# Optimization experiments

Hardware: AMD Instinct MI355X
Metric: run time of the kernel (lower is better)

Reference implementation:

```python
import jax, jax.numpy as jnp
import numpy as np

N = 50000  # nodes
E = 800000  # edges (avg degree 16)


def gcn_agg(x, senders, receivers, n, add_self_edges):
    """jraph.GraphConvolution aggregation with symmetric normalization.
    x: [n, d] node feats already passed through update_node_fn."""
    if add_self_edges:
        idx = jnp.arange(n, dtype=senders.dtype)
        s = jnp.concatenate([senders, idx])
        r = jnp.concatenate([receivers, idx])
    else:
        s, r = senders, receivers
    ones = jnp.ones(s.shape, x.dtype)
    sdeg = jax.ops.segment_sum(ones, s, num_segments=n)
    rdeg = jax.ops.segment_sum(ones, r, num_segments=n)
    x = x * jax.lax.rsqrt(jnp.maximum(sdeg, 1.0))[:, None]
    x = jax.ops.segment_sum(x[s], r, num_segments=n)  # [E+,d] gather -> scatter-sum
    return x * jax.lax.rsqrt(jnp.maximum(rdeg, 1.0))[:, None]


def setup_inputs() -> dict:
    key = jax.random.key(0)
    ks = jax.random.split(key, 9)
    d_in, d_h, d_z, d_out = 128, 128, 64, 128

    def w(k, i, o):
        return jax.random.normal(k, (i, o), jnp.float32) / np.float32(np.sqrt(i))

    return {
        "nodes": jax.random.normal(ks[0], (N, d_in), jnp.float32),
        "senders": jax.random.randint(ks[1], (E,), 0, N, jnp.int32),
        "receivers": jax.random.randint(ks[2], (E,), 0, N, jnp.int32),
        "eps": jax.random.normal(ks[3], (N, d_z), jnp.float32),
        "W_h": w(ks[4], d_in, d_h), "b_h": jnp.zeros((d_h,), jnp.float32),
        "W_mu": w(ks[5], d_h, d_z), "b_mu": jnp.zeros((d_z,), jnp.float32),
        "W_ls": w(ks[6], d_h, d_z), "b_ls": jnp.zeros((d_z,), jnp.float32),
        "W_dh": w(ks[7], d_z, d_h), "b_dh": jnp.zeros((d_h,), jnp.float32),
        "W_do": w(ks[8], d_h, d_out), "b_do": jnp.zeros((d_out,), jnp.float32),
    }


def reference(nodes, senders, receivers, eps, W_h, b_h, W_mu, b_mu,
              W_ls, b_ls, W_dh, b_dh, W_do, b_do):
    n = nodes.shape[0]
    # encoder hidden GCN (add_self_edges=True): Linear+elu update, then agg.
    # (the first of the two identical encoder GCN calls in the source is dead
    #  code -- both read the original graph, only the 2nd result is used)
    h = jax.nn.elu(nodes @ W_h + b_h)
    h = gcn_agg(h, senders, receivers, n, True)
    # mean / log_std GCNs (add_self_edges=False)
    mean = gcn_agg(h @ W_mu + b_mu, senders, receivers, n, False)
    log_std = gcn_agg(h @ W_ls + b_ls, senders, receivers, n, False)
    # reparameterization
    z = mean + jnp.exp(log_std) * eps
    # decoder: GCN(self edges, Linear+elu) -> GCN(no self edges, Linear)
    d = jax.nn.elu(z @ W_dh + b_dh)
    d = gcn_agg(d, senders, receivers, n, True)
    out = gcn_agg(d @ W_do + b_do, senders, receivers, n, False)
    return mean, log_std, out
```

## Files before the change

### kernel.cpp

```cpp
#include <hip/hip_runtime.h>
#include <hip/hip_bf16.h>
#include <hip/hip_fp16.h>
#include <math.h>


typedef _Float16 f16x8 __attribute__((ext_vector_type(8)));
typedef float    f32x4 __attribute__((ext_vector_type(4)));

#define HSL 128
#define HIST_LDS_W 12544

__global__ __launch_bounds__(256)
void hist8_k(const int* __restrict__ snd, const int* __restrict__ rcv,
             unsigned int* __restrict__ partial, int nE, int nW)
{
    __shared__ unsigned int sh[HIST_LDS_W];
    const int slice = blockIdx.x, arr = blockIdx.y;
    const int* __restrict__ idx = arr ? rcv : snd;
    for (int w = threadIdx.x; w < nW; w += 256) sh[w] = 0u;
    __syncthreads();
    const int per = (nE + HSL - 1) / HSL;
    const int e1 = min(nE, slice * per + per);
    for (int e = slice * per + threadIdx.x; e < e1; e += 256) {
        int v = idx[e];
        atomicAdd(&sh[v >> 2], 1u << ((v & 3) * 8));
    }
    __syncthreads();
    unsigned int* dst = partial + ((size_t)arr * HSL + slice) * nW;
    for (int w = threadIdx.x; w < nW; w += 256) dst[w] = sh[w];
}

__global__ __launch_bounds__(256)
void hist8_reduce_k(const unsigned int* __restrict__ partial, int* __restrict__ rdeg,
                    float* __restrict__ dsi, float* __restrict__ dri,
                    float* __restrict__ dsn, float* __restrict__ drn,
                    int n, int nW)
{
    int gid = blockIdx.x * 256 + threadIdx.x;
    if (gid >= 2 * nW) return;
    const int arr = gid / nW, w = gid % nW;
    const unsigned int* src = partial + (size_t)arr * HSL * nW + w;
    int c0 = 0, c1 = 0, c2 = 0, c3 = 0;
    for (int s = 0; s < HSL; ++s) {
        unsigned int v = src[(size_t)s * nW];
        c0 += v & 255u; c1 += (v >> 8) & 255u; c2 += (v >> 16) & 255u; c3 += v >> 24;
    }
    const int cc[4] = {c0, c1, c2, c3};
    const int node0 = w * 4;
#pragma unroll
    for (int u = 0; u < 4; ++u) {
        int node = node0 + u;
        if (node >= n) break;
        float fd = (float)cc[u];
        if (arr == 0) {
            dsi[node] = rsqrtf(fd + 1.0f);
            dsn[node] = rsqrtf(fmaxf(fd, 1.0f));
        } else {
            rdeg[node] = cc[u];
            dri[node] = rsqrtf(fd + 1.0f);
            drn[node] = rsqrtf(fmaxf(fd, 1.0f));
        }
    }
}

__global__ __launch_bounds__(256)
void scan_part_k(const int* __restrict__ deg, int* __restrict__ partial, int n)
{
    __shared__ int sh[256];
    const int t = threadIdx.x;
    const int i = blockIdx.x * 1024 + t * 4;
    int s = 0;
    if (i + 3 < n) { int4 v = *(const int4*)&deg[i]; s = v.x + v.y + v.z + v.w; }
    else { for (int u = 0; u < 4; u++) if (i + u < n) s += deg[i + u]; }
    sh[t] = s; __syncthreads();
    for (int off = 128; off > 0; off >>= 1) {
        if (t < off) sh[t] += sh[t + off];
        __syncthreads();
    }
    if (t == 0) partial[blockIdx.x] = sh[0];
}

__global__ __launch_bounds__(256)
void scan_mid_k(int* __restrict__ partial, int nb, int* __restrict__ row_start, int n)
{
    __shared__ int sh[256];
    const int t = threadIdx.x;
    int v = (t < nb) ? partial[t] : 0;
    sh[t] = v; __syncthreads();
#pragma unroll
    for (int off = 1; off < 256; off <<= 1) {
        int u = (t >= off) ? sh[t - off] : 0;
        __syncthreads();
        sh[t] += u;
        __syncthreads();
    }
    if (t < nb) partial[t] = sh[t];
    if (t == 255) row_start[n] = sh[255];
}

__global__ __launch_bounds__(256)
void scan_apply_k(const int* __restrict__ deg, const int* __restrict__ partial,
                  int* __restrict__ row_start, int* __restrict__ cursor, int n)
{
    __shared__ int sh[256];
    const int t = threadIdx.x;
    const int b = blockIdx.x;
    const int i = b * 1024 + t * 4;
    const int boff = (b == 0) ? 0 : partial[b - 1];
    int v0 = 0, v1 = 0, v2 = 0, v3 = 0;
    if (i + 3 < n) { int4 v = *(const int4*)&deg[i]; v0 = v.x; v1 = v.y; v2 = v.z; v3 = v.w; }
    else {
        if (i     < n) v0 = deg[i];
        if (i + 1 < n) v1 = deg[i + 1];
        if (i + 2 < n) v2 = deg[i + 2];
        if (i + 3 < n) v3 = deg[i + 3];
    }
    const int ts = v0 + v1 + v2 + v3;
    sh[t] = ts; __syncthreads();
#pragma unroll
    for (int off = 1; off < 256; off <<= 1) {
        int u = (t >= off) ? sh[t - off] : 0;
        __syncthreads();
        sh[t] += u;
        __syncthreads();
    }
    const int excl = boff + sh[t] - ts;
    const int p0 = excl, p1 = p0 + v0, p2 = p1 + v1, p3 = p2 + v2;
    if (i + 3 < n) {
        *(int4*)&row_start[i] = make_int4(p0, p1, p2, p3);
        *(int4*)&cursor[i]    = make_int4(p0, p1, p2, p3);
    } else {
        if (i     < n) { row_start[i]     = p0; cursor[i]     = p0; }
        if (i + 1 < n) { row_start[i + 1] = p1; cursor[i + 1] = p1; }
        if (i + 2 < n) { row_start[i + 2] = p2; cursor[i + 2] = p2; }
        if (i + 3 < n) { row_start[i + 3] = p3; cursor[i + 3] = p3; }
    }
}

__global__ __launch_bounds__(256)
void fill_csr_k(const int* __restrict__ s, const int* __restrict__ r,
                int* __restrict__ cursor, int* __restrict__ csr, int nE)
{
    int e = blockIdx.x * 256 + threadIdx.x;
    if (e < nE) {
        int pos = atomicAdd(&cursor[r[e]], 1);
        csr[pos] = s[e];
    }
}

__global__ __launch_bounds__(256)
void wprep_k(const float* __restrict__ W_h, const float* __restrict__ W_mu,
             const float* __restrict__ W_ls, const float* __restrict__ W_dh,
             const float* __restrict__ W_do,
             const float* __restrict__ b_mu, const float* __restrict__ b_ls,
             __half* __restrict__ WT_h, __half* __restrict__ WT2,
             __half* __restrict__ WT_dh, __half* __restrict__ WT_do,
             float* __restrict__ bias2)
{
    int gid = blockIdx.x * 256 + threadIdx.x;
    if (gid < 16384) {
        int m = gid >> 7, k = gid & 127;
        WT_h[gid] = __float2half(W_h[k * 128 + m]);
    } else if (gid < 32768) {
        int t = gid - 16384; int m = t >> 7, k = t & 127;
        float v = (m < 64) ? W_mu[k * 64 + m] : W_ls[k * 64 + (m - 64)];
        WT2[t] = __float2half(v);
    } else if (gid < 40960) {
        int t = gid - 32768; int m = t >> 6, k = t & 63;
        WT_dh[t] = __float2half(W_dh[k * 128 + m]);
    } else if (gid < 57344) {
        int t = gid - 40960; int m = t >> 7, k = t & 127;
        WT_do[t] = __float2half(W_do[k * 128 + m]);
    } else if (gid < 57472) {
        int c = gid - 57344;
        bias2[c] = (c < 64) ? b_mu[c] : b_ls[c - 64];
    }
}

template<int K, int ELU, typename XT>
__global__ __launch_bounds__(256)
void mgemm_k(const XT* __restrict__ X, const __half* __restrict__ WT,
             const float* __restrict__ Bias, const float* __restrict__ rowscale,
             __half* __restrict__ Y, int nrows)
{
    const int lane = threadIdx.x & 63;
    const int w    = threadIdx.x >> 6;
    const int l15  = lane & 15, l4 = lane >> 4;
    const int rowbase = blockIdx.x * 128 + w * 32;
    if (rowbase >= nrows) return;

    f32x4 acc[2][8];
#pragma unroll
    for (int mt = 0; mt < 2; ++mt)
#pragma unroll
        for (int nt = 0; nt < 8; ++nt)
#pragma unroll
            for (int q = 0; q < 4; ++q) acc[mt][nt][q] = 0.f;

    const int r0 = min(rowbase + l15,      nrows - 1);
    const int r1 = min(rowbase + 16 + l15, nrows - 1);

#pragma unroll
    for (int ks = 0; ks < K / 32; ++ks) {
        const int ko = ks * 32 + l4 * 8;
        f16x8 a0, a1;
        if constexpr (sizeof(XT) == 4) {
            const float4 p0 = *(const float4*)&X[(size_t)r0 * K + ko];
            const float4 p1 = *(const float4*)&X[(size_t)r0 * K + ko + 4];
            const float4 q0 = *(const float4*)&X[(size_t)r1 * K + ko];
            const float4 q1 = *(const float4*)&X[(size_t)r1 * K + ko + 4];
            a0[0] = (_Float16)p0.x; a0[1] = (_Float16)p0.y;
            a0[2] = (_Float16)p0.z; a0[3] = (_Float16)p0.w;
            a0[4] = (_Float16)p1.x; a0[5] = (_Float16)p1.y;
            a0[6] = (_Float16)p1.z; a0[7] = (_Float16)p1.w;
            a1[0] = (_Float16)q0.x; a1[1] = (_Float16)q0.y;
            a1[2] = (_Float16)q0.z; a1[3] = (_Float16)q0.w;
            a1[4] = (_Float16)q1.x; a1[5] = (_Float16)q1.y;
            a1[6] = (_Float16)q1.z; a1[7] = (_Float16)q1.w;
        } else {
            a0 = *(const f16x8*)&X[(size_t)r0 * K + ko];
            a1 = *(const f16x8*)&X[(size_t)r1 * K + ko];
        }
#pragma unroll
        for (int nt = 0; nt < 8; ++nt) {
            const f16x8 b = *(const f16x8*)&WT[(size_t)(nt * 16 + l15) * K + ko];
            acc[0][nt] = __builtin_amdgcn_mfma_f32_16x16x32_f16(a0, b, acc[0][nt], 0, 0, 0);
            acc[1][nt] = __builtin_amdgcn_mfma_f32_16x16x32_f16(a1, b, acc[1][nt], 0, 0, 0);
        }
    }

    float rs[2][4]; int gr[2][4];
#pragma unroll
    for (int mt = 0; mt < 2; ++mt)
#pragma unroll
        for (int i = 0; i < 4; ++i) {
            int g = rowbase + mt * 16 + l4 * 4 + i;
            gr[mt][i] = g;
            rs[mt][i] = (g < nrows) ? rowscale[g] : 0.f;
        }
#pragma unroll
    for (int nt = 0; nt < 8; ++nt) {
        const float bias = Bias[nt * 16 + l15];
#pragma unroll
        for (int mt = 0; mt < 2; ++mt)
#pragma unroll
            for (int i = 0; i < 4; ++i) {
                if (gr[mt][i] < nrows) {
                    float v = acc[mt][nt][i] + bias;
                    if (ELU) v = (v > 0.f) ? v : expm1f(v);
                    Y[(size_t)gr[mt][i] * 128 + nt * 16 + l15] = __float2half(v * rs[mt][i]);
                }
            }
    }
}

__device__ inline void agg_core(const __half* __restrict__ y, const int* __restrict__ csr,
                                int beg, int end, int g, int c16, float (&acc)[8])
{
    int j = beg;
    for (; j + 8 <= end; j += 8) {
        const int s0 = csr[j + g], s1 = csr[j + 4 + g];
        const f16x8 r0 = *(const f16x8*)&y[(size_t)s0 * 128 + c16 * 8];
        const f16x8 r1 = *(const f16x8*)&y[(size_t)s1 * 128 + c16 * 8];
#pragma unroll
        for (int k = 0; k < 8; ++k) acc[k] += (float)r0[k] + (float)r1[k];
    }
    for (; j < end; j += 4) {
        const int e = j + g;
        const bool ok = e < end;
        const int s = csr[ok ? e : end - 1];
        const f16x8 r = *(const f16x8*)&y[(size_t)s * 128 + c16 * 8];
        if (ok) {
#pragma unroll
            for (int k = 0; k < 8; ++k) acc[k] += (float)r[k];
        }
    }
#pragma unroll
    for (int k = 0; k < 8; ++k) {
        acc[k] += __shfl_xor(acc[k], 16);
        acc[k] += __shfl_xor(acc[k], 32);
    }
}

__global__ __launch_bounds__(256)
void aggw_self_k(const __half* __restrict__ y, const int* __restrict__ row_start,
                 const int* __restrict__ csr, const float* __restrict__ rsc,
                 __half* __restrict__ out, int n)
{
    const int v    = (blockIdx.x * 256 + threadIdx.x) >> 6;
    const int lane = threadIdx.x & 63;
    if (v >= n) return;
    const int g = lane >> 4, c16 = lane & 15;
    const int beg = row_start[v], end = row_start[v + 1];

    float acc[8] = {0.f, 0.f, 0.f, 0.f, 0.f, 0.f, 0.f, 0.f};
    if (g == 0) {
        const f16x8 r = *(const f16x8*)&y[(size_t)v * 128 + c16 * 8];
#pragma unroll
        for (int k = 0; k < 8; ++k) acc[k] += (float)r[k];
    }
    agg_core(y, csr, beg, end, g, c16, acc);
    if (g == 0) {
        const float sc = rsc[v];
        f16x8 o;
#pragma unroll
        for (int k = 0; k < 8; ++k) o[k] = (_Float16)(acc[k] * sc);
        *(f16x8*)&out[(size_t)v * 128 + c16 * 8] = o;
    }
}

__global__ __launch_bounds__(256)
void aggw_f32_k(const __half* __restrict__ y, const int* __restrict__ row_start,
                const int* __restrict__ csr, const float* __restrict__ rsc,
                float* __restrict__ out, int n)
{
    const int v    = (blockIdx.x * 256 + threadIdx.x) >> 6;
    const int lane = threadIdx.x & 63;
    if (v >= n) return;
    const int g = lane >> 4, c16 = lane & 15;
    const int beg = row_start[v], end = row_start[v + 1];

    float acc[8] = {0.f, 0.f, 0.f, 0.f, 0.f, 0.f, 0.f, 0.f};
    agg_core(y, csr, beg, end, g, c16, acc);
    const float sc = rsc[v];
    if (g == 0)
        *(float4*)&out[(size_t)v * 128 + c16 * 8] =
            make_float4(acc[0] * sc, acc[1] * sc, acc[2] * sc, acc[3] * sc);
    if (g == 1)
        *(float4*)&out[(size_t)v * 128 + c16 * 8 + 4] =
            make_float4(acc[4] * sc, acc[5] * sc, acc[6] * sc, acc[7] * sc);
}

__global__ __launch_bounds__(256)
void aggw_2z_k(const __half* __restrict__ y, const int* __restrict__ row_start,
               const int* __restrict__ csr, const float* __restrict__ rsc,
               const float* __restrict__ eps,
               float* __restrict__ mean, float* __restrict__ lstd,
               __half* __restrict__ z16, int n)
{
    const int v    = (blockIdx.x * 256 + threadIdx.x) >> 6;
    const int lane = threadIdx.x & 63;
    if (v >= n) return;
    const int g = lane >> 4, c16 = lane & 15;
    const int beg = row_start[v], end = row_start[v + 1];

    float acc[8] = {0.f, 0.f, 0.f, 0.f, 0.f, 0.f, 0.f, 0.f};
    agg_core(y, csr, beg, end, g, c16, acc);
    const float sc = rsc[v];
#pragma unroll
    for (int k = 0; k < 8; ++k) acc[k] *= sc;

    if (c16 < 8) {
        if (g == 0) *(float4*)&mean[(size_t)v * 64 + c16 * 8]     = make_float4(acc[0], acc[1], acc[2], acc[3]);
        if (g == 1) *(float4*)&mean[(size_t)v * 64 + c16 * 8 + 4] = make_float4(acc[4], acc[5], acc[6], acc[7]);
    } else {
        if (g == 0) *(float4*)&lstd[(size_t)v * 64 + (c16 - 8) * 8]     = make_float4(acc[0], acc[1], acc[2], acc[3]);
        if (g == 1) *(float4*)&lstd[(size_t)v * 64 + (c16 - 8) * 8 + 4] = make_float4(acc[4], acc[5], acc[6], acc[7]);
    }
    float lsv[8];
#pragma unroll
    for (int k = 0; k < 8; ++k) lsv[k] = __shfl_xor(acc[k], 8);
    if (g == 0 && c16 < 8) {
        const float4 e0 = *(const float4*)&eps[(size_t)v * 64 + c16 * 8];
        const float4 e1 = *(const float4*)&eps[(size_t)v * 64 + c16 * 8 + 4];
        const float ev[8] = {e0.x, e0.y, e0.z, e0.w, e1.x, e1.y, e1.z, e1.w};
        f16x8 o;
#pragma unroll
        for (int k = 0; k < 8; ++k) o[k] = (_Float16)(acc[k] + expf(lsv[k]) * ev[k]);
        *(f16x8*)&z16[(size_t)v * 64 + c16 * 8] = o;
    }
}

extern "C" void kernel_launch(void* const* d_in, const int* in_sizes, int n_in,
                              void* d_out, int out_size, void* d_ws, size_t ws_size,
                              hipStream_t stream)
{
    const float* nodes = (const float*)d_in[0];
    const int*   snd   = (const int*)d_in[1];
    const int*   rcv   = (const int*)d_in[2];
    const float* eps   = (const float*)d_in[3];
    const float* W_h  = (const float*)d_in[4];  const float* b_h  = (const float*)d_in[5];
    const float* W_mu = (const float*)d_in[6];  const float* b_mu = (const float*)d_in[7];
    const float* W_ls = (const float*)d_in[8];  const float* b_ls = (const float*)d_in[9];
    const float* W_dh = (const float*)d_in[10]; const float* b_dh = (const float*)d_in[11];
    const float* W_do = (const float*)d_in[12]; const float* b_do = (const float*)d_in[13];

    const int n  = in_sizes[0] / 128;
    const int nE = in_sizes[1];
    const int nW = (n + 3) >> 2;

    __half* bufA16 = (__half*)d_ws;
    __half* bufB16 = bufA16 + (size_t)n * 128;
    __half* bufC16 = bufB16 + (size_t)n * 128;
    float* dsi = (float*)(bufC16 + (size_t)n * 64);
    float* dri = dsi + n;
    float* dsn = dri + n;
    float* drn = dsn + n;
    int* rdeg      = (int*)(drn + n);
    int* row_start = rdeg + n;
    int* cursor    = row_start + n + 4;
    int* spart     = cursor + n;
    int* csr       = spart + 256;
    __half* WT_h  = (__half*)(csr + nE);
    __half* WT2   = WT_h + 16384;
    __half* WT_dh = WT2 + 16384;
    __half* WT_do = WT_dh + 8192;
    float*  bias2 = (float*)(WT_do + 16384);
    unsigned int* partial = (unsigned int*)bufA16;

    float* mean = (float*)d_out;
    float* lstd = mean + (size_t)n * 64;
    float* outp = lstd + (size_t)n * 64;

    auto cdiv = [](int a, int b) { return (a + b - 1) / b; };
    const int gE = cdiv(nE, 256);
    const int gG = cdiv(n, 128);
    const int gW = cdiv(n * 64, 256);
    const int nb = cdiv(n, 1024);

    wprep_k<<<cdiv(57472, 256), 256, 0, stream>>>(W_h, W_mu, W_ls, W_dh, W_do,
                                                  b_mu, b_ls, WT_h, WT2, WT_dh, WT_do, bias2);
    hist8_k<<<dim3(HSL, 2), 256, 0, stream>>>(snd, rcv, partial, nE, nW);
    hist8_reduce_k<<<cdiv(2 * nW, 256), 256, 0, stream>>>(partial, rdeg, dsi, dri, dsn, drn, n, nW);
    scan_part_k<<<nb, 256, 0, stream>>>(rdeg, spart, n);
    scan_mid_k<<<1, 256, 0, stream>>>(spart, nb, row_start, n);
    scan_apply_k<<<nb, 256, 0, stream>>>(rdeg, spart, row_start, cursor, n);
    fill_csr_k<<<gE, 256, 0, stream>>>(snd, rcv, cursor, csr, nE);

    mgemm_k<128, 1, float><<<gG, 256, 0, stream>>>(nodes, WT_h, b_h, dsi, bufA16, n);
    aggw_self_k<<<gW, 256, 0, stream>>>(bufA16, row_start, csr, dri, bufB16, n);

    mgemm_k<128, 0, __half><<<gG, 256, 0, stream>>>(bufB16, WT2, bias2, dsn, bufA16, n);
    aggw_2z_k<<<gW, 256, 0, stream>>>(bufA16, row_start, csr, drn, eps, mean, lstd, bufC16, n);

    mgemm_k<64, 1, __half><<<gG, 256, 0, stream>>>(bufC16, WT_dh, b_dh, dsi, bufA16, n);
    aggw_self_k<<<gW, 256, 0, stream>>>(bufA16, row_start, csr, dri, bufB16, n);

    mgemm_k<128, 0, __half><<<gG, 256, 0, stream>>>(bufB16, WT_do, b_do, dsn, bufA16, n);
    aggw_f32_k<<<gW, 256, 0, stream>>>(bufA16, row_start, csr, drn, outp, n);
}
```

Baseline: 330.2 us.

## Build CSR via two-level bucketed counting sort instead of global atomics

Replaces the receiver-side histogram and the global-atomic CSR fill with a two-pass bucketed sort. Edges are first scattered into per-256-node buckets using slice-local shared-memory cursors, then each bucket is counted and locally sorted in LDS before being written contiguously to the CSR. The goal is to remove contention on global atomics and the scattered writes of the old fill kernel. In exchange it adds several kernel launches and a staging buffer with a fixed per-bucket capacity (CAP) that silently drops edges if a bucket overflows.

```diff
diff --git a/kernel.cpp b/kernel.cpp
--- a/kernel.cpp
+++ b/kernel.cpp
@@ -7,39 +7,38 @@
 typedef _Float16 f16x8 __attribute__((ext_vector_type(8)));
 typedef float    f32x4 __attribute__((ext_vector_type(4)));
 
-#define HSL 128
+#define HSL 64
 #define HIST_LDS_W 12544
-
-__global__ __launch_bounds__(256)
-void hist8_k(const int* __restrict__ snd, const int* __restrict__ rcv,
-             unsigned int* __restrict__ partial, int nE, int nW)
+#define NSLICE 256
+#define CAP 8000
+
+__global__ __launch_bounds__(256)
+void hist8s_k(const int* __restrict__ snd, unsigned int* __restrict__ partial,
+              int nE, int nW)
 {
     __shared__ unsigned int sh[HIST_LDS_W];
-    const int slice = blockIdx.x, arr = blockIdx.y;
-    const int* __restrict__ idx = arr ? rcv : snd;
+    const int slice = blockIdx.x;
     for (int w = threadIdx.x; w < nW; w += 256) sh[w] = 0u;
     __syncthreads();
     const int per = (nE + HSL - 1) / HSL;
     const int e1 = min(nE, slice * per + per);
     for (int e = slice * per + threadIdx.x; e < e1; e += 256) {
-        int v = idx[e];
+        int v = snd[e];
         atomicAdd(&sh[v >> 2], 1u << ((v & 3) * 8));
     }
     __syncthreads();
-    unsigned int* dst = partial + ((size_t)arr * HSL + slice) * nW;
+    unsigned int* dst = partial + (size_t)slice * nW;
     for (int w = threadIdx.x; w < nW; w += 256) dst[w] = sh[w];
 }
 
 __global__ __launch_bounds__(256)
-void hist8_reduce_k(const unsigned int* __restrict__ partial, int* __restrict__ rdeg,
-                    float* __restrict__ dsi, float* __restrict__ dri,
-                    float* __restrict__ dsn, float* __restrict__ drn,
-                    int n, int nW)
-{
-    int gid = blockIdx.x * 256 + threadIdx.x;
-    if (gid >= 2 * nW) return;
-    const int arr = gid / nW, w = gid % nW;
-    const unsigned int* src = partial + (size_t)arr * HSL * nW + w;
+void hist8s_reduce_k(const unsigned int* __restrict__ partial,
+                     float* __restrict__ dsi, float* __restrict__ dsn,
+                     int n, int nW)
+{
+    int w = blockIdx.x * 256 + threadIdx.x;
+    if (w >= nW) return;
+    const unsigned int* src = partial + w;
     int c0 = 0, c1 = 0, c2 = 0, c3 = 0;
     for (int s = 0; s < HSL; ++s) {
         unsigned int v = src[(size_t)s * nW];
@@ -52,15 +51,109 @@
         int node = node0 + u;
         if (node >= n) break;
         float fd = (float)cc[u];
-        if (arr == 0) {
-            dsi[node] = rsqrtf(fd + 1.0f);
-            dsn[node] = rsqrtf(fmaxf(fd, 1.0f));
-        } else {
-            rdeg[node] = cc[u];
-            dri[node] = rsqrtf(fd + 1.0f);
-            drn[node] = rsqrtf(fmaxf(fd, 1.0f));
-        }
-    }
+        dsi[node] = rsqrtf(fd + 1.0f);
+        dsn[node] = rsqrtf(fmaxf(fd, 1.0f));
+    }
+}
+
+__global__ __launch_bounds__(256)
+void rcount_k(const int* __restrict__ rcv, int* __restrict__ cnt, int nE, int nb)
+{
+    __shared__ int lc[256];
+    const int s = blockIdx.x;
+    if (threadIdx.x < nb) lc[threadIdx.x] = 0;
+    __syncthreads();
+    const int per = (nE + NSLICE - 1) / NSLICE;
+    const int e1 = min(nE, (s + 1) * per);
+    for (int e = s * per + threadIdx.x; e < e1; e += 256)
+        atomicAdd(&lc[rcv[e] >> 8], 1);
+    __syncthreads();
+    if (threadIdx.x < nb) cnt[s * nb + threadIdx.x] = lc[threadIdx.x];
+}
+
+__global__ __launch_bounds__(256)
+void rscan_k(const int* __restrict__ cnt, int* __restrict__ sbase,
+             int* __restrict__ btot, int nb)
+{
+    __shared__ int sh[256];
+    const int b = blockIdx.x, t = threadIdx.x;
+    int v = cnt[t * nb + b];
+    sh[t] = v; __syncthreads();
+#pragma unroll
+    for (int off = 1; off < 256; off <<= 1) {
+        int u = (t >= off) ? sh[t - off] : 0;
+        __syncthreads(); sh[t] += u; __syncthreads();
+    }
+    sbase[t * nb + b] = sh[t] - v;
+    if (t == 255) btot[b] = sh[255];
+}
+
+__global__ __launch_bounds__(256)
+void rscatter_k(const int* __restrict__ snd, const int* __restrict__ rcv,
+                const int* __restrict__ sbase, int2* __restrict__ stage,
+                int nE, int nb)
+{
+    __shared__ int cur[256];
+    const int s = blockIdx.x;
+    if (threadIdx.x < nb) cur[threadIdx.x] = sbase[s * nb + threadIdx.x];
+    __syncthreads();
+    const int per = (nE + NSLICE - 1) / NSLICE;
+    const int e1 = min(nE, (s + 1) * per);
+    for (int e = s * per + threadIdx.x; e < e1; e += 256) {
+        int r = rcv[e], b = r >> 8;
+        int t = atomicAdd(&cur[b], 1);
+        if (t < CAP) stage[(size_t)b * CAP + t] = make_int2(snd[e], r);
+    }
+}
+
+__global__ __launch_bounds__(256)
+void rdeg_k(const int2* __restrict__ stage, const int* __restrict__ btot,
+            int* __restrict__ rdeg, float* __restrict__ dri,
+            float* __restrict__ drn, int n)
+{
+    __shared__ int cnt[256];
+    const int b = blockIdx.x;
+    cnt[threadIdx.x] = 0;
+    __syncthreads();
+    const int tot = min(btot[b], CAP);
+    const int2* sp = stage + (size_t)b * CAP;
+    for (int i = threadIdx.x; i < tot; i += 256)
+        atomicAdd(&cnt[sp[i].y & 255], 1);
+    __syncthreads();
+    const int v = b * 256 + threadIdx.x;
+    if (v < n) {
+        int c = cnt[threadIdx.x];
+        rdeg[v] = c;
+        float fd = (float)c;
+        dri[v] = rsqrtf(fd + 1.0f);
+        drn[v] = rsqrtf(fmaxf(fd, 1.0f));
+    }
+}
+
+__global__ __launch_bounds__(256)
+void rsort_k(const int2* __restrict__ stage, const int* __restrict__ btot,
+             const int* __restrict__ row_start, int* __restrict__ csr, int n)
+{
+    __shared__ int loc[256];
+    __shared__ int lbuf[CAP];
+    const int b = blockIdx.x;
+    const int v0 = b * 256;
+    const int bstart = row_start[v0 < n ? v0 : n];
+    {
+        int v = v0 + threadIdx.x;
+        loc[threadIdx.x] = row_start[v < n ? v : n] - bstart;
+    }
+    __syncthreads();
+    const int tot = min(btot[b], CAP);
+    const int2* sp = stage + (size_t)b * CAP;
+    for (int i = threadIdx.x; i < tot; i += 256) {
+        int2 p = sp[i];
+        int t = atomicAdd(&loc[p.y & 255], 1);
+        if (t < CAP) lbuf[t] = p.x;
+    }
+    __syncthreads();
+    for (int i = threadIdx.x; i < tot; i += 256)
+        csr[bstart + i] = lbuf[i];
 }
 
 __global__ __launch_bounds__(256)
@@ -100,7 +193,7 @@
 
 __global__ __launch_bounds__(256)
 void scan_apply_k(const int* __restrict__ deg, const int* __restrict__ partial,
-                  int* __restrict__ row_start, int* __restrict__ cursor, int n)
+                  int* __restrict__ row_start, int n)
 {
     __shared__ int sh[256];
     const int t = threadIdx.x;
@@ -128,23 +221,11 @@
     const int p0 = excl, p1 = p0 + v0, p2 = p1 + v1, p3 = p2 + v2;
     if (i + 3 < n) {
         *(int4*)&row_start[i] = make_int4(p0, p1, p2, p3);
-        *(int4*)&cursor[i]    = make_int4(p0, p1, p2, p3);
     } else {
-        if (i     < n) { row_start[i]     = p0; cursor[i]     = p0; }
-        if (i + 1 < n) { row_start[i + 1] = p1; cursor[i + 1] = p1; }
-        if (i + 2 < n) { row_start[i + 2] = p2; cursor[i + 2] = p2; }
-        if (i + 3 < n) { row_start[i + 3] = p3; cursor[i + 3] = p3; }
-    }
-}
-
-__global__ __launch_bounds__(256)
-void fill_csr_k(const int* __restrict__ s, const int* __restrict__ r,
-                int* __restrict__ cursor, int* __restrict__ csr, int nE)
-{
-    int e = blockIdx.x * 256 + threadIdx.x;
-    if (e < nE) {
-        int pos = atomicAdd(&cursor[r[e]], 1);
-        csr[pos] = s[e];
+        if (i     < n) row_start[i]     = p0;
+        if (i + 1 < n) row_start[i + 1] = p1;
+        if (i + 2 < n) row_start[i + 2] = p2;
+        if (i + 3 < n) row_start[i + 3] = p3;
     }
 }
 
@@ -388,6 +469,7 @@
     const int n  = in_sizes[0] / 128;
     const int nE = in_sizes[1];
     const int nW = (n + 3) >> 2;
+    const int nb = (n + 255) >> 8;
 
     __half* bufA16 = (__half*)d_ws;
     __half* bufB16 = bufA16 + (size_t)n * 128;
@@ -398,34 +480,40 @@
     float* drn = dsn + n;
     int* rdeg      = (int*)(drn + n);
     int* row_start = rdeg + n;
-    int* cursor    = row_start + n + 4;
-    int* spart     = cursor + n;
+    int* spart     = row_start + n + 4;
     int* csr       = spart + 256;
-    __half* WT_h  = (__half*)(csr + nE);
+    int* cnt       = csr + nE;
+    int* sbase     = cnt + 256 * nb;
+    int* btot      = sbase + 256 * nb;
+    __half* WT_h  = (__half*)(btot + 256);
     __half* WT2   = WT_h + 16384;
     __half* WT_dh = WT2 + 16384;
     __half* WT_do = WT_dh + 8192;
     float*  bias2 = (float*)(WT_do + 16384);
     unsigned int* partial = (unsigned int*)bufA16;
+    int2* stage = (int2*)bufB16;
 
     float* mean = (float*)d_out;
     float* lstd = mean + (size_t)n * 64;
     float* outp = lstd + (size_t)n * 64;
 
     auto cdiv = [](int a, int b) { return (a + b - 1) / b; };
-    const int gE = cdiv(nE, 256);
     const int gG = cdiv(n, 128);
     const int gW = cdiv(n * 64, 256);
-    const int nb = cdiv(n, 1024);
+    const int sb = cdiv(n, 1024);
 
     wprep_k<<<cdiv(57472, 256), 256, 0, stream>>>(W_h, W_mu, W_ls, W_dh, W_do,
                                                   b_mu, b_ls, WT_h, WT2, WT_dh, WT_do, bias2);
-    hist8_k<<<dim3(HSL, 2), 256, 0, stream>>>(snd, rcv, partial, nE, nW);
-    hist8_reduce_k<<<cdiv(2 * nW, 256), 256, 0, stream>>>(partial, rdeg, dsi, dri, dsn, drn, n, nW);
-    scan_part_k<<<nb, 256, 0, stream>>>(rdeg, spart, n);
-    scan_mid_k<<<1, 256, 0, stream>>>(spart, nb, row_start, n);
-    scan_apply_k<<<nb, 256, 0, stream>>>(rdeg, spart, row_start, cursor, n);
-    fill_csr_k<<<gE, 256, 0, stream>>>(snd, rcv, cursor, csr, nE);
+    hist8s_k<<<HSL, 256, 0, stream>>>(snd, partial, nE, nW);
+    hist8s_reduce_k<<<cdiv(nW, 256), 256, 0, stream>>>(partial, dsi, dsn, n, nW);
+    rcount_k<<<NSLICE, 256, 0, stream>>>(rcv, cnt, nE, nb);
+    rscan_k<<<nb, 256, 0, stream>>>(cnt, sbase, btot, nb);
+    rscatter_k<<<NSLICE, 256, 0, stream>>>(snd, rcv, sbase, stage, nE, nb);
+    rdeg_k<<<nb, 256, 0, stream>>>(stage, btot, rdeg, dri, drn, n);
+    scan_part_k<<<sb, 256, 0, stream>>>(rdeg, spart, n);
+    scan_mid_k<<<1, 256, 0, stream>>>(spart, sb, row_start, n);
+    scan_apply_k<<<sb, 256, 0, stream>>>(rdeg, spart, row_start, n);
+    rsort_k<<<nb, 256, 0, stream>>>(stage, btot, row_start, csr, n);
 
     mgemm_k<128, 1, float><<<gG, 256, 0, stream>>>(nodes, WT_h, b_h, dsi, bufA16, n);
     aggw_self_k<<<gW, 256, 0, stream>>>(bufA16, row_start, csr, dri, bufB16, n);
```

Result: faster. 309.8 us (-6.2%).
